# Performance work log

Hardware: AMD Instinct MI355X
Metric: run time of the kernel (lower is better)

## Reference

```python
import jax, jax.numpy as jnp
import numpy as np

N = 8192
HID = 64
TAU = 0.8
LAMBDA = 0.5
POS_DENSITY = 0.005


def setup_inputs() -> dict:
    key = jax.random.key(0)
    k1, k2, k3, k4, k5, k6, k7 = jax.random.split(key, 7)
    x1 = jax.random.normal(k1, (N, HID), dtype=jnp.float32)
    x2 = jax.random.normal(k2, (N, HID), dtype=jnp.float32)
    # xavier_uniform with gain=1.414 for square [HID, HID] linears
    limit = 1.414 * np.sqrt(6.0 / (HID + HID))
    W1 = jax.random.uniform(k3, (HID, HID), dtype=jnp.float32, minval=-limit, maxval=limit)
    b1 = jnp.zeros((HID,), dtype=jnp.float32)
    W2 = jax.random.uniform(k4, (HID, HID), dtype=jnp.float32, minval=-limit, maxval=limit)
    b2 = jnp.zeros((HID,), dtype=jnp.float32)
    pm = (jax.random.uniform(k5, (N, N), dtype=jnp.float32) < POS_DENSITY).astype(jnp.float32)
    positive_matrix = jnp.maximum(pm, jnp.eye(N, dtype=jnp.float32))
    return {"x1": x1, "x2": x2, "W1": W1, "b1": b1, "W2": W2, "b2": b2,
            "positive_matrix": positive_matrix}


def _project(x, W1, b1, W2, b2):
    # nn.Linear(hidden, hidden) -> ELU -> nn.Linear(hidden, hidden)
    h = jax.nn.elu(x @ W1.T + b1)
    return h @ W2.T + b2


def _l2norm(z, eps=1e-12):
    # F.normalize(p=2, dim=1): x / max(||x||, eps)
    n = jnp.linalg.norm(z, axis=-1, keepdims=True)
    return z / jnp.maximum(n, eps)


def _sim(z1, z2, tau):
    return jnp.exp((_l2norm(z1) @ _l2norm(z2).T) / tau)  # [N, N]


def _masked_loss(sim_mat, pos):
    row = sim_mat / (jnp.sum(sim_mat, axis=-1, keepdims=True) + 1e-8)
    return -jnp.log(jnp.sum(row * pos, axis=-1) + 1e-8).mean()


def reference(x1, x2, W1, b1, W2, b2, positive_matrix):
    z1 = _project(x1, W1, b1, W2, b2)
    z2 = _project(x2, W1, b1, W2, b2)
    sc_mp = _sim(z1, z2, TAU)
    mp_sc = _sim(z2, z1, TAU)
    sc_loss = _masked_loss(sc_mp, positive_matrix)
    mp_loss = _masked_loss(mp_sc, positive_matrix)
    return sc_loss * LAMBDA + mp_loss * (1.0 - LAMBDA)
```

## Files before the change

### kernel.cpp

```cpp
#include <hip/hip_runtime.h>
#include <hip/hip_bf16.h>

#define N 8192
#define HID 64
#define JC 16

typedef __attribute__((ext_vector_type(4))) float f32x4;
typedef __attribute__((ext_vector_type(8))) __bf16 bf16x8;

__global__ __launch_bounds__(256) void proj_kernel(
    const float* __restrict__ x1, const float* __restrict__ x2,
    const float* __restrict__ W1, const float* __restrict__ b1,
    const float* __restrict__ W2, const float* __restrict__ b2,
    __bf16* __restrict__ Z1h, __bf16* __restrict__ Z2h)
{
  __shared__ __align__(16) float w1s[64*68];
  __shared__ __align__(16) float w2s[64*68];
  __shared__ __align__(16) float xs[4][64];
  __shared__ __align__(16) float hs[4][64];

  const int tid  = threadIdx.x;
  const int lane = tid & 63;
  const int w    = tid >> 6;

  for (int idx = tid; idx < 64*64; idx += 256) {
    int j = idx >> 6, k = idx & 63;
    w1s[j*68+k] = W1[idx];
    w2s[j*68+k] = W2[idx];
  }
  __syncthreads();

  const float bias1 = b1[lane];
  const float bias2 = b2[lane];

  const int wave_global = blockIdx.x * 4 + w;
  #pragma unroll 1
  for (int it = 0; it < 4; ++it) {
    int R = wave_global * 4 + it;
    const float* src; __bf16* dst;
    if (R < N) { src = x1 + (size_t)R*HID;      dst = Z1h + (size_t)R*HID; }
    else       { src = x2 + (size_t)(R-N)*HID;  dst = Z2h + (size_t)(R-N)*HID; }

    float xv = src[lane];
    xs[w][lane] = xv;
    float acc = bias1;
    #pragma unroll
    for (int qq = 0; qq < 16; ++qq) {
      f32x4 xq = *(const f32x4*)&xs[w][qq*4];
      f32x4 wq = *(const f32x4*)&w1s[lane*68 + qq*4];
      acc += xq.x*wq.x + xq.y*wq.y + xq.z*wq.z + xq.w*wq.w;
    }
    float h = acc > 0.f ? acc : expm1f(acc);
    hs[w][lane] = h;
    float acc2 = bias2;
    #pragma unroll
    for (int qq = 0; qq < 16; ++qq) {
      f32x4 hq = *(const f32x4*)&hs[w][qq*4];
      f32x4 wq = *(const f32x4*)&w2s[lane*68 + qq*4];
      acc2 += hq.x*wq.x + hq.y*wq.y + hq.z*wq.z + hq.w*wq.w;
    }
    float z = acc2;
    float ss = z*z;
    #pragma unroll
    for (int m = 1; m < 64; m <<= 1) ss += __shfl_xor(ss, m);
    float inv = 1.0f / fmaxf(sqrtf(ss), 1e-12f);
    dst[lane] = (__bf16)(z * inv);
  }
}

__global__ __launch_bounds__(256, 4) void sim_kernel(
    const __bf16* __restrict__ Z1h, const __bf16* __restrict__ Z2h,
    const float* __restrict__ pos,
    float* __restrict__ rowsum1, float* __restrict__ num1,
    float* __restrict__ rowsum2, float* __restrict__ num2)
{
  const int tid  = threadIdx.x;
  const int lane = tid & 63;
  const int w    = tid >> 6;
  const int r16  = lane & 15;
  const int q    = lane >> 4;

  const int bi = blockIdx.x / JC;
  const int jc = blockIdx.x % JC;
  const int i0 = bi*64 + w*16;

  const __bf16* z1r = Z1h + (size_t)(i0 + r16)*HID + q*8;
  const __bf16* z2r = Z2h + (size_t)(i0 + r16)*HID + q*8;
  bf16x8 a1lo = *(const bf16x8*)(z1r);
  bf16x8 a1hi = *(const bf16x8*)(z1r + 32);
  bf16x8 a2lo = *(const bf16x8*)(z2r);
  bf16x8 a2hi = *(const bf16x8*)(z2r + 32);

  float s1[4] = {0.f,0.f,0.f,0.f}, n1[4] = {0.f,0.f,0.f,0.f};
  float s2[4] = {0.f,0.f,0.f,0.f}, n2[4] = {0.f,0.f,0.f,0.f};

  const int jbeg = jc * (N/JC);
  const int jend = jbeg + (N/JC);
  const float Cexp = 1.8033688011112042f;

  const float* prow0 = pos + (size_t)(i0 + q*4 + 0)*N + 4*r16;
  const float* prow1 = pos + (size_t)(i0 + q*4 + 1)*N + 4*r16;
  const float* prow2 = pos + (size_t)(i0 + q*4 + 2)*N + 4*r16;
  const float* prow3 = pos + (size_t)(i0 + q*4 + 3)*N + 4*r16;

  const __bf16* z2b = Z2h + (size_t)(4*r16)*HID + q*8;
  const __bf16* z1b = Z1h + (size_t)(4*r16)*HID + q*8;

  #pragma unroll 1
  for (int j0 = jbeg; j0 < jend; j0 += 64) {
    f32x4 pq0 = *(const f32x4*)(prow0 + j0);
    f32x4 pq1 = *(const f32x4*)(prow1 + j0);
    f32x4 pq2 = *(const f32x4*)(prow2 + j0);
    f32x4 pq3 = *(const f32x4*)(prow3 + j0);

    bf16x8 b2l[4], b2h[4], b1l[4], b1h[4];
    #pragma unroll
    for (int c = 0; c < 4; ++c) {
      const __bf16* p2 = z2b + (size_t)(j0 + c)*HID;
      const __bf16* p1 = z1b + (size_t)(j0 + c)*HID;
      b2l[c] = *(const bf16x8*)(p2);
      b2h[c] = *(const bf16x8*)(p2 + 32);
      b1l[c] = *(const bf16x8*)(p1);
      b1h[c] = *(const bf16x8*)(p1 + 32);
    }

    const f32x4 zero4 = {0.f,0.f,0.f,0.f};
    #pragma unroll
    for (int c = 0; c < 4; ++c) {
      f32x4 d1 = __builtin_amdgcn_mfma_f32_16x16x32_bf16(a1lo, b2l[c], zero4, 0,0,0);
      d1       = __builtin_amdgcn_mfma_f32_16x16x32_bf16(a1hi, b2h[c], d1,    0,0,0);
      f32x4 d2 = __builtin_amdgcn_mfma_f32_16x16x32_bf16(a2lo, b1l[c], zero4, 0,0,0);
      d2       = __builtin_amdgcn_mfma_f32_16x16x32_bf16(a2hi, b1h[c], d2,    0,0,0);
      float pv[4] = {pq0[c], pq1[c], pq2[c], pq3[c]};
      #pragma unroll
      for (int r = 0; r < 4; ++r) {
        float e1 = exp2f(d1[r] * Cexp);
        float e2 = exp2f(d2[r] * Cexp);
        s1[r] += e1; n1[r] += e1 * pv[r];
        s2[r] += e2; n2[r] += e2 * pv[r];
      }
    }
  }

  #pragma unroll
  for (int r = 0; r < 4; ++r) {
    #pragma unroll
    for (int m = 1; m < 16; m <<= 1) {
      s1[r] += __shfl_xor(s1[r], m);
      n1[r] += __shfl_xor(n1[r], m);
      s2[r] += __shfl_xor(s2[r], m);
      n2[r] += __shfl_xor(n2[r], m);
    }
  }
  if (r16 == 0) {
    #pragma unroll
    for (int r = 0; r < 4; ++r) {
      int row = i0 + q*4 + r;
      atomicAdd(&rowsum1[row], s1[r]);
      atomicAdd(&num1[row],    n1[r]);
      atomicAdd(&rowsum2[row], s2[r]);
      atomicAdd(&num2[row],    n2[r]);
    }
  }
}

__global__ __launch_bounds__(1024) void loss_kernel(
    const float* __restrict__ rowsum1, const float* __restrict__ num1,
    const float* __restrict__ rowsum2, const float* __restrict__ num2,
    float* __restrict__ out)
{
  __shared__ float part[16];
  const int tid = threadIdx.x, lane = tid & 63, w = tid >> 6;
  float acc = 0.f;
  for (int i = tid; i < N; i += 1024) {
    float sc = -logf(num1[i]/(rowsum1[i]+1e-8f) + 1e-8f);
    float mp = -logf(num2[i]/(rowsum2[i]+1e-8f) + 1e-8f);
    acc += 0.5f*sc + 0.5f*mp;
  }
  #pragma unroll
  for (int m = 1; m < 64; m <<= 1) acc += __shfl_xor(acc, m);
  if (lane == 0) part[w] = acc;
  __syncthreads();
  if (tid == 0) {
    float t = 0.f;
    #pragma unroll
    for (int k = 0; k < 16; ++k) t += part[k];
    out[0] = t * (1.0f/N);
  }
}

extern "C" void kernel_launch(void* const* d_in, const int* in_sizes, int n_in,
                              void* d_out, int out_size, void* d_ws, size_t ws_size,
                              hipStream_t stream) {
  const float* x1  = (const float*)d_in[0];
  const float* x2  = (const float*)d_in[1];
  const float* W1  = (const float*)d_in[2];
  const float* b1  = (const float*)d_in[3];
  const float* W2  = (const float*)d_in[4];
  const float* b2  = (const float*)d_in[5];
  const float* pos = (const float*)d_in[6];

  char* ws = (char*)d_ws;
  __bf16* Z1h = (__bf16*)ws;
  __bf16* Z2h = (__bf16*)(ws + (size_t)N*HID*sizeof(__bf16));
  size_t zbytes = (size_t)2*N*HID*sizeof(__bf16);
  float* rowsum1 = (float*)(ws + zbytes);
  float* num1    = rowsum1 + N;
  float* rowsum2 = num1 + N;
  float* num2    = rowsum2 + N;

  hipMemsetAsync(ws + zbytes, 0, (size_t)4*N*sizeof(float), stream);
  proj_kernel<<<1024, 256, 0, stream>>>(x1, x2, W1, b1, W2, b2, Z1h, Z2h);
  sim_kernel<<<128*JC, 256, 0, stream>>>(Z1h, Z2h, pos, rowsum1, num1, rowsum2, num2);
  loss_kernel<<<1, 1024, 0, stream>>>(rowsum1, num1, rowsum2, num2, (float*)d_out);
}
```

Measured before the change: 449.9 us.

## Split sim kernel into sparse positive scan and dense LDS-tiled rowsum

```diff
diff --git a/kernel.cpp b/kernel.cpp
--- a/kernel.cpp
+++ b/kernel.cpp
@@ -3,7 +3,8 @@
 
 #define N 8192
 #define HID 64
-#define JC 16
+#define RJC 8
+#define QCAP 2048
 
 typedef __attribute__((ext_vector_type(4))) float f32x4;
 typedef __attribute__((ext_vector_type(8))) __bf16 bf16x8;
@@ -68,20 +69,82 @@
   }
 }
 
-__global__ __launch_bounds__(256, 4) void sim_kernel(
+__device__ __forceinline__ void process_pair(
+    int f, const __bf16* __restrict__ Z1h, const __bf16* __restrict__ Z2h,
+    float* __restrict__ num1, float* __restrict__ num2)
+{
+  const float Cexp = 1.8033688011112042f;
+  int i = f >> 13, j = f & (N-1);
+  const __bf16* a1 = Z1h + (size_t)i*HID;
+  const __bf16* b2 = Z2h + (size_t)j*HID;
+  const __bf16* a2 = Z2h + (size_t)i*HID;
+  const __bf16* b1 = Z1h + (size_t)j*HID;
+  float d1 = 0.f, d2 = 0.f;
+  #pragma unroll
+  for (int c = 0; c < 8; ++c) {
+    bf16x8 va1 = *(const bf16x8*)(a1 + c*8);
+    bf16x8 vb2 = *(const bf16x8*)(b2 + c*8);
+    bf16x8 va2 = *(const bf16x8*)(a2 + c*8);
+    bf16x8 vb1 = *(const bf16x8*)(b1 + c*8);
+    #pragma unroll
+    for (int e = 0; e < 8; ++e) {
+      d1 += (float)va1[e] * (float)vb2[e];
+      d2 += (float)va2[e] * (float)vb1[e];
+    }
+  }
+  atomicAdd(&num1[i], exp2f(d1 * Cexp));
+  atomicAdd(&num2[i], exp2f(d2 * Cexp));
+}
+
+__global__ __launch_bounds__(256) void scan_kernel(
+    const float* __restrict__ pos,
     const __bf16* __restrict__ Z1h, const __bf16* __restrict__ Z2h,
-    const float* __restrict__ pos,
-    float* __restrict__ rowsum1, float* __restrict__ num1,
-    float* __restrict__ rowsum2, float* __restrict__ num2)
-{
+    float* __restrict__ num1, float* __restrict__ num2)
+{
+  __shared__ int q_cnt;
+  __shared__ int q_idx[QCAP];
+  const int tid = threadIdx.x;
+  if (tid == 0) q_cnt = 0;
+  __syncthreads();
+
+  const size_t base = (size_t)blockIdx.x * 32768;
+  #pragma unroll 2
+  for (int it = 0; it < 32; ++it) {
+    size_t off = base + (size_t)it*1024 + (size_t)tid*4;
+    f32x4 v = *(const f32x4*)(pos + off);
+    if (v.x != 0.f || v.y != 0.f || v.z != 0.f || v.w != 0.f) {
+      #pragma unroll
+      for (int c = 0; c < 4; ++c) {
+        float vc = (c==0)?v.x:(c==1)?v.y:(c==2)?v.z:v.w;
+        if (vc != 0.f) {
+          int slot = atomicAdd(&q_cnt, 1);
+          if (slot < QCAP) q_idx[slot] = (int)off + c;
+          else process_pair((int)off + c, Z1h, Z2h, num1, num2);
+        }
+      }
+    }
+  }
+  __syncthreads();
+  int cnt = min(q_cnt, QCAP);
+  for (int k = tid; k < cnt; k += 256)
+    process_pair(q_idx[k], Z1h, Z2h, num1, num2);
+}
+
+__global__ __launch_bounds__(256) void rowsum_kernel(
+    const __bf16* __restrict__ Z1h, const __bf16* __restrict__ Z2h,
+    float* __restrict__ rowsum1, float* __restrict__ rowsum2)
+{
+  __shared__ __align__(16) __bf16 s1[64*72];
+  __shared__ __align__(16) __bf16 s2[64*72];
+
   const int tid  = threadIdx.x;
   const int lane = tid & 63;
   const int w    = tid >> 6;
   const int r16  = lane & 15;
   const int q    = lane >> 4;
 
-  const int bi = blockIdx.x / JC;
-  const int jc = blockIdx.x % JC;
+  const int bi = blockIdx.x / RJC;
+  const int jc = blockIdx.x % RJC;
   const int i0 = bi*64 + w*16;
 
   const __bf16* z1r = Z1h + (size_t)(i0 + r16)*HID + q*8;
@@ -91,53 +154,41 @@
   bf16x8 a2lo = *(const bf16x8*)(z2r);
   bf16x8 a2hi = *(const bf16x8*)(z2r + 32);
 
-  float s1[4] = {0.f,0.f,0.f,0.f}, n1[4] = {0.f,0.f,0.f,0.f};
-  float s2[4] = {0.f,0.f,0.f,0.f}, n2[4] = {0.f,0.f,0.f,0.f};
-
-  const int jbeg = jc * (N/JC);
-  const int jend = jbeg + (N/JC);
+  float sa1[4] = {0.f,0.f,0.f,0.f}, sa2[4] = {0.f,0.f,0.f,0.f};
   const float Cexp = 1.8033688011112042f;
 
-  const float* prow0 = pos + (size_t)(i0 + q*4 + 0)*N + 4*r16;
-  const float* prow1 = pos + (size_t)(i0 + q*4 + 1)*N + 4*r16;
-  const float* prow2 = pos + (size_t)(i0 + q*4 + 2)*N + 4*r16;
-  const float* prow3 = pos + (size_t)(i0 + q*4 + 3)*N + 4*r16;
-
-  const __bf16* z2b = Z2h + (size_t)(4*r16)*HID + q*8;
-  const __bf16* z1b = Z1h + (size_t)(4*r16)*HID + q*8;
+  const int jbeg = jc * (N/RJC);
+  const int jend = jbeg + (N/RJC);
+
+  const int c0 = tid,       r0 = c0 >> 3, e0 = (c0 & 7) * 8;
+  const int c1 = tid + 256, r1 = c1 >> 3, e1 = (c1 & 7) * 8;
 
   #pragma unroll 1
   for (int j0 = jbeg; j0 < jend; j0 += 64) {
-    f32x4 pq0 = *(const f32x4*)(prow0 + j0);
-    f32x4 pq1 = *(const f32x4*)(prow1 + j0);
-    f32x4 pq2 = *(const f32x4*)(prow2 + j0);
-    f32x4 pq3 = *(const f32x4*)(prow3 + j0);
-
-    bf16x8 b2l[4], b2h[4], b1l[4], b1h[4];
+    __syncthreads();
+    *(uint4*)&s1[r0*72 + e0] = *(const uint4*)(Z1h + (size_t)(j0 + r0)*HID + e0);
+    *(uint4*)&s1[r1*72 + e1] = *(const uint4*)(Z1h + (size_t)(j0 + r1)*HID + e1);
+    *(uint4*)&s2[r0*72 + e0] = *(const uint4*)(Z2h + (size_t)(j0 + r0)*HID + e0);
+    *(uint4*)&s2[r1*72 + e1] = *(const uint4*)(Z2h + (size_t)(j0 + r1)*HID + e1);
+    __syncthreads();
+
+    const f32x4 zero4 = {0.f,0.f,0.f,0.f};
     #pragma unroll
     for (int c = 0; c < 4; ++c) {
-      const __bf16* p2 = z2b + (size_t)(j0 + c)*HID;
-      const __bf16* p1 = z1b + (size_t)(j0 + c)*HID;
-      b2l[c] = *(const bf16x8*)(p2);
-      b2h[c] = *(const bf16x8*)(p2 + 32);
-      b1l[c] = *(const bf16x8*)(p1);
-      b1h[c] = *(const bf16x8*)(p1 + 32);
-    }
-
-    const f32x4 zero4 = {0.f,0.f,0.f,0.f};
-    #pragma unroll
-    for (int c = 0; c < 4; ++c) {
-      f32x4 d1 = __builtin_amdgcn_mfma_f32_16x16x32_bf16(a1lo, b2l[c], zero4, 0,0,0);
-      d1       = __builtin_amdgcn_mfma_f32_16x16x32_bf16(a1hi, b2h[c], d1,    0,0,0);
-      f32x4 d2 = __builtin_amdgcn_mfma_f32_16x16x32_bf16(a2lo, b1l[c], zero4, 0,0,0);
-      d2       = __builtin_amdgcn_mfma_f32_16x16x32_bf16(a2hi, b1h[c], d2,    0,0,0);
-      float pv[4] = {pq0[c], pq1[c], pq2[c], pq3[c]};
+      const __bf16* p2 = &s2[(c*16 + r16)*72 + q*8];
+      const __bf16* p1 = &s1[(c*16 + r16)*72 + q*8];
+      bf16x8 b2lo = *(const bf16x8*)(p2);
+      bf16x8 b2hi = *(const bf16x8*)(p2 + 32);
+      bf16x8 b1lo = *(const bf16x8*)(p1);
+      bf16x8 b1hi = *(const bf16x8*)(p1 + 32);
+      f32x4 d1 = __builtin_amdgcn_mfma_f32_16x16x32_bf16(a1lo, b2lo, zero4, 0,0,0);
+      d1       = __builtin_amdgcn_mfma_f32_16x16x32_bf16(a1hi, b2hi, d1,    0,0,0);
+      f32x4 d2 = __builtin_amdgcn_mfma_f32_16x16x32_bf16(a2lo, b1lo, zero4, 0,0,0);
+      d2       = __builtin_amdgcn_mfma_f32_16x16x32_bf16(a2hi, b1hi, d2,    0,0,0);
       #pragma unroll
       for (int r = 0; r < 4; ++r) {
-        float e1 = exp2f(d1[r] * Cexp);
-        float e2 = exp2f(d2[r] * Cexp);
-        s1[r] += e1; n1[r] += e1 * pv[r];
-        s2[r] += e2; n2[r] += e2 * pv[r];
+        sa1[r] += exp2f(d1[r] * Cexp);
+        sa2[r] += exp2f(d2[r] * Cexp);
       }
     }
   }
@@ -146,20 +197,16 @@
   for (int r = 0; r < 4; ++r) {
     #pragma unroll
     for (int m = 1; m < 16; m <<= 1) {
-      s1[r] += __shfl_xor(s1[r], m);
-      n1[r] += __shfl_xor(n1[r], m);
-      s2[r] += __shfl_xor(s2[r], m);
-      n2[r] += __shfl_xor(n2[r], m);
+      sa1[r] += __shfl_xor(sa1[r], m);
+      sa2[r] += __shfl_xor(sa2[r], m);
     }
   }
   if (r16 == 0) {
     #pragma unroll
     for (int r = 0; r < 4; ++r) {
       int row = i0 + q*4 + r;
-      atomicAdd(&rowsum1[row], s1[r]);
-      atomicAdd(&num1[row],    n1[r]);
-      atomicAdd(&rowsum2[row], s2[r]);
-      atomicAdd(&num2[row],    n2[r]);
+      atomicAdd(&rowsum1[row], sa1[r]);
+      atomicAdd(&rowsum2[row], sa2[r]);
     }
   }
 }
@@ -211,6 +258,7 @@
 
   hipMemsetAsync(ws + zbytes, 0, (size_t)4*N*sizeof(float), stream);
   proj_kernel<<<1024, 256, 0, stream>>>(x1, x2, W1, b1, W2, b2, Z1h, Z2h);
-  sim_kernel<<<128*JC, 256, 0, stream>>>(Z1h, Z2h, pos, rowsum1, num1, rowsum2, num2);
+  scan_kernel<<<2048, 256, 0, stream>>>(pos, Z1h, Z2h, num1, num2);
+  rowsum_kernel<<<128*RJC, 256, 0, stream>>>(Z1h, Z2h, rowsum1, rowsum2);
   loss_kernel<<<1, 1024, 0, stream>>>(rowsum1, num1, rowsum2, num2, (float*)d_out);
 }
```

New measurement: 536.3 us. +19.2%, slower.
